# Kernel tuning notes

Hardware: AMD Instinct MI355X
Metric: run time of the kernel (lower is better)

## Reference

```python
import jax, jax.numpy as jnp
import numpy as np

B, T, ND, SD, H = 4096, 256, 16, 8, 64
IN = SD + ND  # LSTM input dim


def setup_inputs() -> dict:
    key = jax.random.key(0)
    ks = jax.random.split(key, 20)
    def w(k, shape):
        fan_in = shape[0]
        return jax.random.normal(k, shape, jnp.float32) / np.sqrt(fan_in)
    return {
        "noise": jax.random.normal(ks[0], (B, T - 1, ND), jnp.float32),
        "eps": jax.random.normal(ks[1], (B, T - 1, SD), jnp.float32),
        "Wx": w(ks[2], (IN, 4 * H)),
        "Wh": w(ks[3], (H, 4 * H)),
        "b": jnp.zeros((4 * H,), jnp.float32),
        "Wm1": w(ks[4], (H, H)), "bm1": jnp.zeros((H,), jnp.float32),
        "Wm2": w(ks[5], (H, H)), "bm2": jnp.zeros((H,), jnp.float32),
        "Wm3": w(ks[6], (H, SD)), "bm3": jnp.zeros((SD,), jnp.float32),
        "Wv1": w(ks[7], (H, H)), "bv1": jnp.zeros((H,), jnp.float32),
        "Wv2": w(ks[8], (H, H)), "bv2": jnp.zeros((H,), jnp.float32),
        "Wv3": w(ks[9], (H, SD)), "bv3": jnp.zeros((SD,), jnp.float32),
    }


def reference(noise, eps, Wx, Wh, b, Wm1, bm1, Wm2, bm2, Wm3, bm3,
              Wv1, bv1, Wv2, bv2, Wv3, bv3):
    Bn = noise.shape[0]
    Hn = Wh.shape[0]
    Dn = Wm3.shape[1]

    def mlp(h, W1, b1, W2, b2, W3, b3):
        a = jax.nn.relu(h @ W1 + b1)
        a = jax.nn.relu(a @ W2 + b2)
        return a @ W3 + b3

    def step(carry, inp_t):
        x, h, c = carry
        n_t, e_t = inp_t
        # Keras LSTM: gates ordered i, f, g(cell), o
        z = jnp.concatenate([x, n_t], axis=-1) @ Wx + h @ Wh + b  # [B, 4H]
        i, f, g, o = jnp.split(z, 4, axis=-1)
        c = jax.nn.sigmoid(f) * c + jax.nn.sigmoid(i) * jnp.tanh(g)
        h = jax.nn.sigmoid(o) * jnp.tanh(c)
        mu = mlp(h, Wm1, bm1, Wm2, bm2, Wm3, bm3)
        std = jnp.exp(0.5 * mlp(h, Wv1, bv1, Wv2, bv2, Wv3, bv3))
        x = mu + std * e_t  # reparameterized Normal(mu, std).sample()
        return (x, h, c), x

    x0 = jnp.zeros((Bn, Dn), noise.dtype)  # log_series=True -> zeros
    h0 = jnp.zeros((Bn, Hn), noise.dtype)
    c0 = jnp.zeros((Bn, Hn), noise.dtype)
    noise_t = jnp.swapaxes(noise, 0, 1)  # [T-1, B, ND]
    eps_t = jnp.swapaxes(eps, 0, 1)      # [T-1, B, SD]
    _, xs = jax.lax.scan(step, (x0, h0, c0), (noise_t, eps_t))
    seq = jnp.concatenate([x0[:, None, :], jnp.swapaxes(xs, 0, 1)], axis=1)  # [B, T, SD]
    return jnp.cumsum(seq, axis=1)
```

## Files before the change

kernel.cpp:

```cpp
#include <hip/hip_runtime.h>

typedef _Float16 half8 __attribute__((ext_vector_type(8)));
typedef _Float16 half4 __attribute__((ext_vector_type(4)));
typedef unsigned short ushort8 __attribute__((ext_vector_type(8)));
typedef float f32x4 __attribute__((ext_vector_type(4)));

#define TSTEPS 255
#define R 16
#define BLK 512
#define XSH 104
#define ZS 260
#define ASH 72

__device__ __forceinline__ float frcp(float x) { return __builtin_amdgcn_rcpf(x); }

__device__ __forceinline__ f32x4 mfma16(half8 a, half8 b, f32x4 c) {
  return __builtin_amdgcn_mfma_f32_16x16x32_f16(a, b, c, 0, 0, 0);
}

__device__ __forceinline__ unsigned int packhl(float x) {
  _Float16 hh = (_Float16)x;
  _Float16 hl = (_Float16)(x - (float)hh);
  return (unsigned int)__builtin_bit_cast(unsigned short, hh) |
         ((unsigned int)__builtin_bit_cast(unsigned short, hl) << 16);
}

__global__ __launch_bounds__(BLK)
void genlstm_kernel(const float* __restrict__ noise,
                    const float* __restrict__ eps,
                    const float* __restrict__ Wx,
                    const float* __restrict__ Wh,
                    const float* __restrict__ bg,
                    const float* __restrict__ Wm1, const float* __restrict__ bm1,
                    const float* __restrict__ Wm2, const float* __restrict__ bm2,
                    const float* __restrict__ Wm3, const float* __restrict__ bm3,
                    const float* __restrict__ Wv1, const float* __restrict__ bv1,
                    const float* __restrict__ Wv2, const float* __restrict__ bv2,
                    const float* __restrict__ Wv3, const float* __restrict__ bv3,
                    float* __restrict__ out)
{
  __shared__ __align__(16) _Float16 xh[R][XSH];
  __shared__ __align__(16) _Float16 xl[R][XSH];
  __shared__ __align__(16) float    z2[R][ZS];
  __shared__ __align__(16) _Float16 a1h[2][R][ASH];
  __shared__ __align__(16) _Float16 a1l[2][R][ASH];
  __shared__ __align__(16) _Float16 a2h[2][R][ASH];
  __shared__ __align__(16) _Float16 a2l[2][R][ASH];

  const int tid  = threadIdx.x;
  const int w    = tid >> 6;
  const int l    = tid & 63;
  const int lrow = l & 15;
  const int lq   = l >> 4;
  const long rowbase = (long)blockIdx.x * R;

  half8 gBhi[2][3], gBlo[2][3];
  #pragma unroll
  for (int t = 0; t < 2; ++t)
    #pragma unroll
    for (int kt = 0; kt < 3; ++kt)
      #pragma unroll
      for (int j = 0; j < 8; ++j) {
        int k  = 32 * kt + 8 * lq + j;
        int jc = 32 * w + 16 * t + lrow;
        int n  = 64 * (jc & 3) + (jc >> 2);
        float v = 0.f;
        if (k < 64) v = Wh[k * 256 + n];
        else if (k < 88) v = Wx[(k - 64) * 256 + n];
        _Float16 h = (_Float16)v;
        gBhi[t][kt][j] = h;
        gBlo[t][kt][j] = (_Float16)(v - (float)h);
      }

  const int chain = w >> 2;
  const int nt = w & 3;
  const float* W1 = chain ? Wv1 : Wm1;
  const float* W2 = chain ? Wv2 : Wm2;
  half8 B1hi[2], B1lo[2], B2hi[2], B2lo[2];
  #pragma unroll
  for (int kt = 0; kt < 2; ++kt)
    #pragma unroll
    for (int j = 0; j < 8; ++j) {
      int k = 32 * kt + 8 * lq + j;
      int n = 16 * nt + lrow;
      float v1 = W1[k * 64 + n];
      _Float16 h1 = (_Float16)v1;
      B1hi[kt][j] = h1; B1lo[kt][j] = (_Float16)(v1 - (float)h1);
      float v2 = W2[k * 64 + n];
      _Float16 h2 = (_Float16)v2;
      B2hi[kt][j] = h2; B2lo[kt][j] = (_Float16)(v2 - (float)h2);
    }

  half8 Amhi[2], Amlo[2], Avhi[2], Avlo[2];
  #pragma unroll
  for (int kt = 0; kt < 2; ++kt)
    #pragma unroll
    for (int j = 0; j < 8; ++j) {
      int k = 32 * kt + 8 * lq + j;
      float vm = (lrow < 8) ? Wm3[k * 8 + lrow] : 0.f;
      _Float16 hm = (_Float16)vm;
      Amhi[kt][j] = hm; Amlo[kt][j] = (_Float16)(vm - (float)hm);
      float vv = (lrow < 8) ? Wv3[k * 8 + lrow] : 0.f;
      _Float16 hv = (_Float16)vv;
      Avhi[kt][j] = hv; Avlo[kt][j] = (_Float16)(vv - (float)hv);
    }

  const float bias1 = (chain ? bv1 : bm1)[16 * nt + lrow];
  const float bias2 = (chain ? bv2 : bm2)[16 * nt + lrow];

  const int d0 = 4 * (lq & 1);
  const float4 bm3q = *(const float4*)&bm3[d0];
  const float4 bv3q = *(const float4*)&bv3[d0];

  const float4 bgq = {bg[l], bg[64 + l], bg[128 + l], bg[192 + l]};

  float cst0 = 0.f, cst1 = 0.f;

  f32x4 cum4 = {0.f, 0.f, 0.f, 0.f};
  float4 ep4 = {0.f, 0.f, 0.f, 0.f};
  unsigned int pk0 = 0, pk1 = 0, pk2 = 0, pk3 = 0;

  half8 hHi[2], hLo[2];
  #pragma unroll
  for (int kt = 0; kt < 2; ++kt)
    #pragma unroll
    for (int j = 0; j < 8; ++j) { hHi[kt][j] = (_Float16)0; hLo[kt][j] = (_Float16)0; }

  for (int i = tid; i < R * XSH; i += BLK) {
    (&xh[0][0])[i] = (_Float16)0;
    (&xl[0][0])[i] = (_Float16)0;
  }
  {
    const int r5 = tid >> 3, d5 = tid & 7;
    if (tid < 128) out[((rowbase + r5) * 256) * 8 + d5] = 0.f;
  }

  float4 nz = {0.f, 0.f, 0.f, 0.f};
  if (tid < 64) {
    int r = tid >> 2, j4 = (tid & 3) * 4;
    float4 n0 = *(const float4*)&noise[((rowbase + r) * TSTEPS) * 16 + j4];
    float tmp[4] = {n0.x, n0.y, n0.z, n0.w};
    half4 nh, nl;
    #pragma unroll
    for (int j = 0; j < 4; ++j) {
      _Float16 h = (_Float16)tmp[j];
      nh[j] = h; nl[j] = (_Float16)(tmp[j] - (float)h);
    }
    *(half4*)&xh[r][72 + j4] = nh;
    *(half4*)&xl[r][72 + j4] = nl;
    nz = *(const float4*)&noise[((rowbase + r) * TSTEPS + 1) * 16 + j4];
  }
  if (lq < 2) ep4 = *(const float4*)&eps[((rowbase + lrow) * TSTEPS) * 8 + d0];
  __syncthreads();

  for (int ts = 0; ts < TSTEPS; ++ts) {
    half8 Xhi = *(const half8*)&xh[lrow][64 + 8 * lq];
    half8 Xlo = *(const half8*)&xl[lrow][64 + 8 * lq];
    {
      unsigned int up0 = (unsigned int)__shfl_down((int)pk0, 16);
      unsigned int up1 = (unsigned int)__shfl_down((int)pk1, 16);
      unsigned int up2 = (unsigned int)__shfl_down((int)pk2, 16);
      unsigned int up3 = (unsigned int)__shfl_down((int)pk3, 16);
      if (lq == 0) {
        ushort8 uh, ul;
        uh[0] = (unsigned short)pk0; ul[0] = (unsigned short)(pk0 >> 16);
        uh[1] = (unsigned short)pk1; ul[1] = (unsigned short)(pk1 >> 16);
        uh[2] = (unsigned short)pk2; ul[2] = (unsigned short)(pk2 >> 16);
        uh[3] = (unsigned short)pk3; ul[3] = (unsigned short)(pk3 >> 16);
        uh[4] = (unsigned short)up0; ul[4] = (unsigned short)(up0 >> 16);
        uh[5] = (unsigned short)up1; ul[5] = (unsigned short)(up1 >> 16);
        uh[6] = (unsigned short)up2; ul[6] = (unsigned short)(up2 >> 16);
        uh[7] = (unsigned short)up3; ul[7] = (unsigned short)(up3 >> 16);
        Xhi = __builtin_bit_cast(half8, uh);
        Xlo = __builtin_bit_cast(half8, ul);
      }
    }

    f32x4 accz0 = {0.f, 0.f, 0.f, 0.f};
    f32x4 accz1 = {0.f, 0.f, 0.f, 0.f};
    accz0 = mfma16(hHi[0], gBhi[0][0], accz0);
    accz1 = mfma16(hHi[0], gBhi[1][0], accz1);
    accz0 = mfma16(hLo[0], gBhi[0][0], accz0);
    accz1 = mfma16(hLo[0], gBhi[1][0], accz1);
    accz0 = mfma16(hHi[0], gBlo[0][0], accz0);
    accz1 = mfma16(hHi[0], gBlo[1][0], accz1);
    accz0 = mfma16(hHi[1], gBhi[0][1], accz0);
    accz1 = mfma16(hHi[1], gBhi[1][1], accz1);
    accz0 = mfma16(hLo[1], gBhi[0][1], accz0);
    accz1 = mfma16(hLo[1], gBhi[1][1], accz1);
    accz0 = mfma16(hHi[1], gBlo[0][1], accz0);
    accz1 = mfma16(hHi[1], gBlo[1][1], accz1);
    accz0 = mfma16(Xhi, gBhi[0][2], accz0);
    accz1 = mfma16(Xhi, gBhi[1][2], accz1);
    accz0 = mfma16(Xlo, gBhi[0][2], accz0);
    accz1 = mfma16(Xlo, gBhi[1][2], accz1);
    accz0 = mfma16(Xhi, gBlo[0][2], accz0);
    accz1 = mfma16(Xhi, gBlo[1][2], accz1);
    {
      const int r0 = 4 * lq;
      #pragma unroll
      for (int k = 0; k < 4; ++k) {
        z2[r0 + k][32 * w + lrow]      = accz0[k];
        z2[r0 + k][32 * w + 16 + lrow] = accz1[k];
      }
    }
    __syncthreads();

    #pragma unroll
    for (int rr = 0; rr < 2; ++rr) {
      const int r = w + rr * 8;
      float4 zq = *(const float4*)&z2[r][4 * l];
      float zi = zq.x + bgq.x;
      float zf = zq.y + bgq.y;
      float zg = zq.z + bgq.z;
      float zo = zq.w + bgq.w;
      float si = frcp(1.f + __expf(-zi));
      float sf = frcp(1.f + __expf(-zf));
      float so = frcp(1.f + __expf(-zo));
      float ag = fabsf(zg), eg = __expf(-2.f * ag);
      float tg = copysignf((1.f - eg) * frcp(1.f + eg), zg);
      float cs = rr ? cst1 : cst0;
      cs = fmaf(sf, cs, si * tg);
      if (rr) cst1 = cs; else cst0 = cs;
      float ac = fabsf(cs), ec = __expf(-2.f * ac);
      float tc = copysignf((1.f - ec) * frcp(1.f + ec), cs);
      float hv = so * tc;
      _Float16 hh = (_Float16)hv;
      xh[r][l] = hh;
      xl[r][l] = (_Float16)(hv - (float)hh);
    }
    if (tid < 64) {
      int r = tid >> 2, j4 = (tid & 3) * 4;
      float tmp[4] = {nz.x, nz.y, nz.z, nz.w};
      half4 nh, nl;
      #pragma unroll
      for (int j = 0; j < 4; ++j) {
        _Float16 h = (_Float16)tmp[j];
        nh[j] = h; nl[j] = (_Float16)(tmp[j] - (float)h);
      }
      *(half4*)&xh[r][72 + j4] = nh;
      *(half4*)&xl[r][72 + j4] = nl;
      if (ts + 2 < TSTEPS)
        nz = *(const float4*)&noise[((rowbase + r) * TSTEPS + ts + 2) * 16 + j4];
    }
    __syncthreads();

    {
      hHi[0] = *(const half8*)&xh[lrow][8 * lq];
      hHi[1] = *(const half8*)&xh[lrow][32 + 8 * lq];
      hLo[0] = *(const half8*)&xl[lrow][8 * lq];
      hLo[1] = *(const half8*)&xl[lrow][32 + 8 * lq];
      f32x4 acc = {0.f, 0.f, 0.f, 0.f};
      #pragma unroll
      for (int kt = 0; kt < 2; ++kt) {
        acc = mfma16(hHi[kt], B1hi[kt], acc);
        acc = mfma16(hLo[kt], B1hi[kt], acc);
        acc = mfma16(hHi[kt], B1lo[kt], acc);
      }
      const int r0 = 4 * lq;
      #pragma unroll
      for (int k = 0; k < 4; ++k) {
        float v = fmaxf(acc[k] + bias1, 0.f);
        _Float16 vh = (_Float16)v;
        a1h[chain][r0 + k][16 * nt + lrow] = vh;
        a1l[chain][r0 + k][16 * nt + lrow] = (_Float16)(v - (float)vh);
      }
    }
    __syncthreads();

    {
      half8 ahi0 = *(const half8*)&a1h[chain][lrow][8 * lq];
      half8 ahi1 = *(const half8*)&a1h[chain][lrow][32 + 8 * lq];
      half8 alo0 = *(const half8*)&a1l[chain][lrow][8 * lq];
      half8 alo1 = *(const half8*)&a1l[chain][lrow][32 + 8 * lq];
      f32x4 acc = {0.f, 0.f, 0.f, 0.f};
      acc = mfma16(ahi0, B2hi[0], acc);
      acc = mfma16(alo0, B2hi[0], acc);
      acc = mfma16(ahi0, B2lo[0], acc);
      acc = mfma16(ahi1, B2hi[1], acc);
      acc = mfma16(alo1, B2hi[1], acc);
      acc = mfma16(ahi1, B2lo[1], acc);
      const int r0 = 4 * lq;
      #pragma unroll
      for (int k = 0; k < 4; ++k) {
        float v = fmaxf(acc[k] + bias2, 0.f);
        _Float16 vh = (_Float16)v;
        a2h[chain][r0 + k][16 * nt + lrow] = vh;
        a2l[chain][r0 + k][16 * nt + lrow] = (_Float16)(v - (float)vh);
      }
    }
    __syncthreads();

    f32x4 accm = {0.f, 0.f, 0.f, 0.f};
    f32x4 accv = {0.f, 0.f, 0.f, 0.f};
    {
      half8 b0h0 = *(const half8*)&a2h[0][lrow][8 * lq];
      half8 b0h1 = *(const half8*)&a2h[0][lrow][32 + 8 * lq];
      half8 b0l0 = *(const half8*)&a2l[0][lrow][8 * lq];
      half8 b0l1 = *(const half8*)&a2l[0][lrow][32 + 8 * lq];
      accm = mfma16(Amhi[0], b0h0, accm);
      accm = mfma16(Amlo[0], b0h0, accm);
      accm = mfma16(Amhi[0], b0l0, accm);
      accm = mfma16(Amhi[1], b0h1, accm);
      accm = mfma16(Amlo[1], b0h1, accm);
      accm = mfma16(Amhi[1], b0l1, accm);
      half8 b1h0 = *(const half8*)&a2h[1][lrow][8 * lq];
      half8 b1h1 = *(const half8*)&a2h[1][lrow][32 + 8 * lq];
      half8 b1l0 = *(const half8*)&a2l[1][lrow][8 * lq];
      half8 b1l1 = *(const half8*)&a2l[1][lrow][32 + 8 * lq];
      accv = mfma16(Avhi[0], b1h0, accv);
      accv = mfma16(Avlo[0], b1h0, accv);
      accv = mfma16(Avhi[0], b1l0, accv);
      accv = mfma16(Avhi[1], b1h1, accv);
      accv = mfma16(Avlo[1], b1h1, accv);
      accv = mfma16(Avhi[1], b1l1, accv);
    }

    {
      float x0v = fmaf(__expf(0.5f * (accv[0] + bv3q.x)), ep4.x, accm[0] + bm3q.x);
      float x1v = fmaf(__expf(0.5f * (accv[1] + bv3q.y)), ep4.y, accm[1] + bm3q.y);
      float x2v = fmaf(__expf(0.5f * (accv[2] + bv3q.z)), ep4.z, accm[2] + bm3q.z);
      float x3v = fmaf(__expf(0.5f * (accv[3] + bv3q.w)), ep4.w, accm[3] + bm3q.w);
      cum4[0] += x0v; cum4[1] += x1v; cum4[2] += x2v; cum4[3] += x3v;
      if (w == 0 && lq < 2) {
        float4 cv = {cum4[0], cum4[1], cum4[2], cum4[3]};
        *(float4*)&out[((rowbase + lrow) * 256 + ts + 1) * 8 + d0] = cv;
      }
      pk0 = packhl(x0v);
      pk1 = packhl(x1v);
      pk2 = packhl(x2v);
      pk3 = packhl(x3v);
      if (ts + 1 < TSTEPS && lq < 2)
        ep4 = *(const float4*)&eps[((rowbase + lrow) * TSTEPS + ts + 1) * 8 + d0];
    }
  }
}

extern "C" void kernel_launch(void* const* d_in, const int* in_sizes, int n_in,
                              void* d_out, int out_size, void* d_ws, size_t ws_size,
                              hipStream_t stream) {
  const float* noise = (const float*)d_in[0];
  const float* eps   = (const float*)d_in[1];
  const float* Wx    = (const float*)d_in[2];
  const float* Wh    = (const float*)d_in[3];
  const float* bg    = (const float*)d_in[4];
  const float* Wm1   = (const float*)d_in[5];
  const float* bm1   = (const float*)d_in[6];
  const float* Wm2   = (const float*)d_in[7];
  const float* bm2   = (const float*)d_in[8];
  const float* Wm3   = (const float*)d_in[9];
  const float* bm3   = (const float*)d_in[10];
  const float* Wv1   = (const float*)d_in[11];
  const float* bv1   = (const float*)d_in[12];
  const float* Wv2   = (const float*)d_in[13];
  const float* bv2   = (const float*)d_in[14];
  const float* Wv3   = (const float*)d_in[15];
  const float* bv3   = (const float*)d_in[16];
  float* out = (float*)d_out;

  dim3 grid(4096 / R), block(BLK);
  hipLaunchKernelGGL(genlstm_kernel, grid, block, 0, stream,
                     noise, eps, Wx, Wh, bg, Wm1, bm1, Wm2, bm2, Wm3, bm3,
                     Wv1, bv1, Wv2, bv2, Wv3, bv3, out);
}
```

Before: 626.2 us.

## Transpose gate matmul so each lane owns full gate quads, drop z2 staging

Swaps the MFMA operand order for the LSTM gate matmul and remaps weight columns so each lane's accumulator holds all four gates (i,f,g,o) for one hidden unit. The cell update can then run directly on the accumulators, which removes the z2 shared-memory round trip and one block barrier per step. The x/noise staging buffer is double-buffered, and only wave 0 computes the output head and writes x back through shared memory instead of using shuffles. The price is an extra barrier at the end of each step and seven idle waves during the head computation.

```diff
diff --git a/kernel.cpp b/kernel.cpp
--- a/kernel.cpp
+++ b/kernel.cpp
@@ -2,27 +2,18 @@
 
 typedef _Float16 half8 __attribute__((ext_vector_type(8)));
 typedef _Float16 half4 __attribute__((ext_vector_type(4)));
-typedef unsigned short ushort8 __attribute__((ext_vector_type(8)));
 typedef float f32x4 __attribute__((ext_vector_type(4)));
 
 #define TSTEPS 255
 #define R 16
 #define BLK 512
 #define XSH 104
-#define ZS 260
 #define ASH 72
 
 __device__ __forceinline__ float frcp(float x) { return __builtin_amdgcn_rcpf(x); }
 
 __device__ __forceinline__ f32x4 mfma16(half8 a, half8 b, f32x4 c) {
   return __builtin_amdgcn_mfma_f32_16x16x32_f16(a, b, c, 0, 0, 0);
-}
-
-__device__ __forceinline__ unsigned int packhl(float x) {
-  _Float16 hh = (_Float16)x;
-  _Float16 hl = (_Float16)(x - (float)hh);
-  return (unsigned int)__builtin_bit_cast(unsigned short, hh) |
-         ((unsigned int)__builtin_bit_cast(unsigned short, hl) << 16);
 }
 
 __global__ __launch_bounds__(BLK)
@@ -39,9 +30,8 @@
                     const float* __restrict__ Wv3, const float* __restrict__ bv3,
                     float* __restrict__ out)
 {
-  __shared__ __align__(16) _Float16 xh[R][XSH];
-  __shared__ __align__(16) _Float16 xl[R][XSH];
-  __shared__ __align__(16) float    z2[R][ZS];
+  __shared__ __align__(16) _Float16 xh[2][R][XSH];
+  __shared__ __align__(16) _Float16 xl[2][R][XSH];
   __shared__ __align__(16) _Float16 a1h[2][R][ASH];
   __shared__ __align__(16) _Float16 a1l[2][R][ASH];
   __shared__ __align__(16) _Float16 a2h[2][R][ASH];
@@ -54,23 +44,24 @@
   const int lq   = l >> 4;
   const long rowbase = (long)blockIdx.x * R;
 
-  half8 gBhi[2][3], gBlo[2][3];
+  half8 gAhi[2][3], gAlo[2][3];
   #pragma unroll
-  for (int t = 0; t < 2; ++t)
+  for (int t = 0; t < 2; ++t) {
+    const int T = 2 * w + t;
+    const int n = 64 * (lrow & 3) + 4 * T + (lrow >> 2);
     #pragma unroll
     for (int kt = 0; kt < 3; ++kt)
       #pragma unroll
       for (int j = 0; j < 8; ++j) {
-        int k  = 32 * kt + 8 * lq + j;
-        int jc = 32 * w + 16 * t + lrow;
-        int n  = 64 * (jc & 3) + (jc >> 2);
+        int k = 32 * kt + 8 * lq + j;
         float v = 0.f;
         if (k < 64) v = Wh[k * 256 + n];
         else if (k < 88) v = Wx[(k - 64) * 256 + n];
         _Float16 h = (_Float16)v;
-        gBhi[t][kt][j] = h;
-        gBlo[t][kt][j] = (_Float16)(v - (float)h);
-      }
+        gAhi[t][kt][j] = h;
+        gAlo[t][kt][j] = (_Float16)(v - (float)h);
+      }
+  }
 
   const int chain = w >> 2;
   const int nt = w & 3;
@@ -108,17 +99,17 @@
   const float bias1 = (chain ? bv1 : bm1)[16 * nt + lrow];
   const float bias2 = (chain ? bv2 : bm2)[16 * nt + lrow];
 
+  const int hc1 = 8 * w + lq, hc2 = hc1 + 4;
+  const float4 bgA = {bg[hc1], bg[64 + hc1], bg[128 + hc1], bg[192 + hc1]};
+  const float4 bgB = {bg[hc2], bg[64 + hc2], bg[128 + hc2], bg[192 + hc2]};
+
   const int d0 = 4 * (lq & 1);
   const float4 bm3q = *(const float4*)&bm3[d0];
   const float4 bv3q = *(const float4*)&bv3[d0];
 
-  const float4 bgq = {bg[l], bg[64 + l], bg[128 + l], bg[192 + l]};
-
   float cst0 = 0.f, cst1 = 0.f;
-
   f32x4 cum4 = {0.f, 0.f, 0.f, 0.f};
   float4 ep4 = {0.f, 0.f, 0.f, 0.f};
-  unsigned int pk0 = 0, pk1 = 0, pk2 = 0, pk3 = 0;
 
   half8 hHi[2], hLo[2];
   #pragma unroll
@@ -126,9 +117,9 @@
     #pragma unroll
     for (int j = 0; j < 8; ++j) { hHi[kt][j] = (_Float16)0; hLo[kt][j] = (_Float16)0; }
 
-  for (int i = tid; i < R * XSH; i += BLK) {
-    (&xh[0][0])[i] = (_Float16)0;
-    (&xl[0][0])[i] = (_Float16)0;
+  for (int i = tid; i < 2 * R * XSH; i += BLK) {
+    (&xh[0][0][0])[i] = (_Float16)0;
+    (&xl[0][0][0])[i] = (_Float16)0;
   }
   {
     const int r5 = tid >> 3, d5 = tid & 7;
@@ -146,88 +137,72 @@
       _Float16 h = (_Float16)tmp[j];
       nh[j] = h; nl[j] = (_Float16)(tmp[j] - (float)h);
     }
-    *(half4*)&xh[r][72 + j4] = nh;
-    *(half4*)&xl[r][72 + j4] = nl;
+    *(half4*)&xh[0][r][72 + j4] = nh;
+    *(half4*)&xl[0][r][72 + j4] = nl;
     nz = *(const float4*)&noise[((rowbase + r) * TSTEPS + 1) * 16 + j4];
   }
-  if (lq < 2) ep4 = *(const float4*)&eps[((rowbase + lrow) * TSTEPS) * 8 + d0];
+  if (w == 0 && lq < 2)
+    ep4 = *(const float4*)&eps[((rowbase + lrow) * TSTEPS) * 8 + d0];
   __syncthreads();
 
   for (int ts = 0; ts < TSTEPS; ++ts) {
-    half8 Xhi = *(const half8*)&xh[lrow][64 + 8 * lq];
-    half8 Xlo = *(const half8*)&xl[lrow][64 + 8 * lq];
+    const int p = ts & 1, p1 = p ^ 1;
+
+    half8 Xhi = *(const half8*)&xh[p][lrow][64 + 8 * lq];
+    half8 Xlo = *(const half8*)&xl[p][lrow][64 + 8 * lq];
+
+    f32x4 az0 = {0.f, 0.f, 0.f, 0.f};
+    f32x4 az1 = {0.f, 0.f, 0.f, 0.f};
+    az0 = mfma16(gAhi[0][0], hHi[0], az0);
+    az1 = mfma16(gAhi[1][0], hHi[0], az1);
+    az0 = mfma16(gAlo[0][0], hHi[0], az0);
+    az1 = mfma16(gAlo[1][0], hHi[0], az1);
+    az0 = mfma16(gAhi[0][0], hLo[0], az0);
+    az1 = mfma16(gAhi[1][0], hLo[0], az1);
+    az0 = mfma16(gAhi[0][1], hHi[1], az0);
+    az1 = mfma16(gAhi[1][1], hHi[1], az1);
+    az0 = mfma16(gAlo[0][1], hHi[1], az0);
+    az1 = mfma16(gAlo[1][1], hHi[1], az1);
+    az0 = mfma16(gAhi[0][1], hLo[1], az0);
+    az1 = mfma16(gAhi[1][1], hLo[1], az1);
+    az0 = mfma16(gAhi[0][2], Xhi, az0);
+    az1 = mfma16(gAhi[1][2], Xhi, az1);
+    az0 = mfma16(gAlo[0][2], Xhi, az0);
+    az1 = mfma16(gAlo[1][2], Xhi, az1);
+    az0 = mfma16(gAhi[0][2], Xlo, az0);
+    az1 = mfma16(gAhi[1][2], Xlo, az1);
+
     {
-      unsigned int up0 = (unsigned int)__shfl_down((int)pk0, 16);
-      unsigned int up1 = (unsigned int)__shfl_down((int)pk1, 16);
-      unsigned int up2 = (unsigned int)__shfl_down((int)pk2, 16);
-      unsigned int up3 = (unsigned int)__shfl_down((int)pk3, 16);
-      if (lq == 0) {
-        ushort8 uh, ul;
-        uh[0] = (unsigned short)pk0; ul[0] = (unsigned short)(pk0 >> 16);
-        uh[1] = (unsigned short)pk1; ul[1] = (unsigned short)(pk1 >> 16);
-        uh[2] = (unsigned short)pk2; ul[2] = (unsigned short)(pk2 >> 16);
-        uh[3] = (unsigned short)pk3; ul[3] = (unsigned short)(pk3 >> 16);
-        uh[4] = (unsigned short)up0; ul[4] = (unsigned short)(up0 >> 16);
-        uh[5] = (unsigned short)up1; ul[5] = (unsigned short)(up1 >> 16);
-        uh[6] = (unsigned short)up2; ul[6] = (unsigned short)(up2 >> 16);
-        uh[7] = (unsigned short)up3; ul[7] = (unsigned short)(up3 >> 16);
-        Xhi = __builtin_bit_cast(half8, uh);
-        Xlo = __builtin_bit_cast(half8, ul);
-      }
-    }
-
-    f32x4 accz0 = {0.f, 0.f, 0.f, 0.f};
-    f32x4 accz1 = {0.f, 0.f, 0.f, 0.f};
-    accz0 = mfma16(hHi[0], gBhi[0][0], accz0);
-    accz1 = mfma16(hHi[0], gBhi[1][0], accz1);
-    accz0 = mfma16(hLo[0], gBhi[0][0], accz0);
-    accz1 = mfma16(hLo[0], gBhi[1][0], accz1);
-    accz0 = mfma16(hHi[0], gBlo[0][0], accz0);
-    accz1 = mfma16(hHi[0], gBlo[1][0], accz1);
-    accz0 = mfma16(hHi[1], gBhi[0][1], accz0);
-    accz1 = mfma16(hHi[1], gBhi[1][1], accz1);
-    accz0 = mfma16(hLo[1], gBhi[0][1], accz0);
-    accz1 = mfma16(hLo[1], gBhi[1][1], accz1);
-    accz0 = mfma16(hHi[1], gBlo[0][1], accz0);
-    accz1 = mfma16(hHi[1], gBlo[1][1], accz1);
-    accz0 = mfma16(Xhi, gBhi[0][2], accz0);
-    accz1 = mfma16(Xhi, gBhi[1][2], accz1);
-    accz0 = mfma16(Xlo, gBhi[0][2], accz0);
-    accz1 = mfma16(Xlo, gBhi[1][2], accz1);
-    accz0 = mfma16(Xhi, gBlo[0][2], accz0);
-    accz1 = mfma16(Xhi, gBlo[1][2], accz1);
-    {
-      const int r0 = 4 * lq;
-      #pragma unroll
-      for (int k = 0; k < 4; ++k) {
-        z2[r0 + k][32 * w + lrow]      = accz0[k];
-        z2[r0 + k][32 * w + 16 + lrow] = accz1[k];
-      }
-    }
-    __syncthreads();
-
-    #pragma unroll
-    for (int rr = 0; rr < 2; ++rr) {
-      const int r = w + rr * 8;
-      float4 zq = *(const float4*)&z2[r][4 * l];
-      float zi = zq.x + bgq.x;
-      float zf = zq.y + bgq.y;
-      float zg = zq.z + bgq.z;
-      float zo = zq.w + bgq.w;
+      float zi = az0[0] + bgA.x, zf = az0[1] + bgA.y;
+      float zg = az0[2] + bgA.z, zo = az0[3] + bgA.w;
       float si = frcp(1.f + __expf(-zi));
       float sf = frcp(1.f + __expf(-zf));
       float so = frcp(1.f + __expf(-zo));
       float ag = fabsf(zg), eg = __expf(-2.f * ag);
       float tg = copysignf((1.f - eg) * frcp(1.f + eg), zg);
-      float cs = rr ? cst1 : cst0;
-      cs = fmaf(sf, cs, si * tg);
-      if (rr) cst1 = cs; else cst0 = cs;
-      float ac = fabsf(cs), ec = __expf(-2.f * ac);
-      float tc = copysignf((1.f - ec) * frcp(1.f + ec), cs);
+      cst0 = fmaf(sf, cst0, si * tg);
+      float ac = fabsf(cst0), ec = __expf(-2.f * ac);
+      float tc = copysignf((1.f - ec) * frcp(1.f + ec), cst0);
       float hv = so * tc;
       _Float16 hh = (_Float16)hv;
-      xh[r][l] = hh;
-      xl[r][l] = (_Float16)(hv - (float)hh);
+      xh[p1][lrow][hc1] = hh;
+      xl[p1][lrow][hc1] = (_Float16)(hv - (float)hh);
+    }
+    {
+      float zi = az1[0] + bgB.x, zf = az1[1] + bgB.y;
+      float zg = az1[2] + bgB.z, zo = az1[3] + bgB.w;
+      float si = frcp(1.f + __expf(-zi));
+      float sf = frcp(1.f + __expf(-zf));
+      float so = frcp(1.f + __expf(-zo));
+      float ag = fabsf(zg), eg = __expf(-2.f * ag);
+      float tg = copysignf((1.f - eg) * frcp(1.f + eg), zg);
+      cst1 = fmaf(sf, cst1, si * tg);
+      float ac = fabsf(cst1), ec = __expf(-2.f * ac);
+      float tc = copysignf((1.f - ec) * frcp(1.f + ec), cst1);
+      float hv = so * tc;
+      _Float16 hh = (_Float16)hv;
+      xh[p1][lrow][hc2] = hh;
+      xl[p1][lrow][hc2] = (_Float16)(hv - (float)hh);
     }
     if (tid < 64) {
       int r = tid >> 2, j4 = (tid & 3) * 4;
@@ -238,18 +213,18 @@
         _Float16 h = (_Float16)tmp[j];
         nh[j] = h; nl[j] = (_Float16)(tmp[j] - (float)h);
       }
-      *(half4*)&xh[r][72 + j4] = nh;
-      *(half4*)&xl[r][72 + j4] = nl;
+      *(half4*)&xh[p1][r][72 + j4] = nh;
+      *(half4*)&xl[p1][r][72 + j4] = nl;
       if (ts + 2 < TSTEPS)
         nz = *(const float4*)&noise[((rowbase + r) * TSTEPS + ts + 2) * 16 + j4];
     }
     __syncthreads();
 
     {
-      hHi[0] = *(const half8*)&xh[lrow][8 * lq];
-      hHi[1] = *(const half8*)&xh[lrow][32 + 8 * lq];
-      hLo[0] = *(const half8*)&xl[lrow][8 * lq];
-      hLo[1] = *(const half8*)&xl[lrow][32 + 8 * lq];
+      hHi[0] = *(const half8*)&xh[p1][lrow][8 * lq];
+      hHi[1] = *(const half8*)&xh[p1][lrow][32 + 8 * lq];
+      hLo[0] = *(const half8*)&xl[p1][lrow][8 * lq];
+      hLo[1] = *(const half8*)&xl[p1][lrow][32 + 8 * lq];
       f32x4 acc = {0.f, 0.f, 0.f, 0.f};
       #pragma unroll
       for (int kt = 0; kt < 2; ++kt) {
@@ -291,13 +266,12 @@
     }
     __syncthreads();
 
-    f32x4 accm = {0.f, 0.f, 0.f, 0.f};
-    f32x4 accv = {0.f, 0.f, 0.f, 0.f};
-    {
+    if (w == 0) {
       half8 b0h0 = *(const half8*)&a2h[0][lrow][8 * lq];
       half8 b0h1 = *(const half8*)&a2h[0][lrow][32 + 8 * lq];
       half8 b0l0 = *(const half8*)&a2l[0][lrow][8 * lq];
       half8 b0l1 = *(const half8*)&a2l[0][lrow][32 + 8 * lq];
+      f32x4 accm = {0.f, 0.f, 0.f, 0.f};
       accm = mfma16(Amhi[0], b0h0, accm);
       accm = mfma16(Amlo[0], b0h0, accm);
       accm = mfma16(Amhi[0], b0l0, accm);
@@ -308,31 +282,36 @@
       half8 b1h1 = *(const half8*)&a2h[1][lrow][32 + 8 * lq];
       half8 b1l0 = *(const half8*)&a2l[1][lrow][8 * lq];
       half8 b1l1 = *(const half8*)&a2l[1][lrow][32 + 8 * lq];
+      f32x4 accv = {0.f, 0.f, 0.f, 0.f};
       accv = mfma16(Avhi[0], b1h0, accv);
       accv = mfma16(Avlo[0], b1h0, accv);
       accv = mfma16(Avhi[0], b1l0, accv);
       accv = mfma16(Avhi[1], b1h1, accv);
       accv = mfma16(Avlo[1], b1h1, accv);
       accv = mfma16(Avhi[1], b1l1, accv);
-    }
-
-    {
-      float x0v = fmaf(__expf(0.5f * (accv[0] + bv3q.x)), ep4.x, accm[0] + bm3q.x);
-      float x1v = fmaf(__expf(0.5f * (accv[1] + bv3q.y)), ep4.y, accm[1] + bm3q.y);
-      float x2v = fmaf(__expf(0.5f * (accv[2] + bv3q.z)), ep4.z, accm[2] + bm3q.z);
-      float x3v = fmaf(__expf(0.5f * (accv[3] + bv3q.w)), ep4.w, accm[3] + bm3q.w);
-      cum4[0] += x0v; cum4[1] += x1v; cum4[2] += x2v; cum4[3] += x3v;
-      if (w == 0 && lq < 2) {
+
+      float xs0 = fmaf(__expf(0.5f * (accv[0] + bv3q.x)), ep4.x, accm[0] + bm3q.x);
+      float xs1 = fmaf(__expf(0.5f * (accv[1] + bv3q.y)), ep4.y, accm[1] + bm3q.y);
+      float xs2 = fmaf(__expf(0.5f * (accv[2] + bv3q.z)), ep4.z, accm[2] + bm3q.z);
+      float xs3 = fmaf(__expf(0.5f * (accv[3] + bv3q.w)), ep4.w, accm[3] + bm3q.w);
+      cum4[0] += xs0; cum4[1] += xs1; cum4[2] += xs2; cum4[3] += xs3;
+      if (lq < 2) {
         float4 cv = {cum4[0], cum4[1], cum4[2], cum4[3]};
         *(float4*)&out[((rowbase + lrow) * 256 + ts + 1) * 8 + d0] = cv;
-      }
-      pk0 = packhl(x0v);
-      pk1 = packhl(x1v);
-      pk2 = packhl(x2v);
-      pk3 = packhl(x3v);
-      if (ts + 1 < TSTEPS && lq < 2)
-        ep4 = *(const float4*)&eps[((rowbase + lrow) * TSTEPS + ts + 1) * 8 + d0];
-    }
+        float xs[4] = {xs0, xs1, xs2, xs3};
+        half4 xhv, xlv;
+        #pragma unroll
+        for (int j = 0; j < 4; ++j) {
+          _Float16 hh = (_Float16)xs[j];
+          xhv[j] = hh; xlv[j] = (_Float16)(xs[j] - (float)hh);
+        }
+        *(half4*)&xh[p1][lrow][64 + d0] = xhv;
+        *(half4*)&xl[p1][lrow][64 + d0] = xlv;
+        if (ts + 1 < TSTEPS)
+          ep4 = *(const float4*)&eps[((rowbase + lrow) * TSTEPS + ts + 1) * 8 + d0];
+      }
+    }
+    __syncthreads();
   }
 }
 
```

Result: faster. 544.7 us (-13.0%).
